# Kernel optimization log

Measured on AMD Instinct MI355X. Metric: run time of the kernel, lower is better.

Reference implementation:

```python
import jax, jax.numpy as jnp
import numpy as np

N_NODES = 50000   # local subgraph nodes
N_ENT   = 100000  # global entity vocab
N_REL   = 16
DIM     = 128
LAYERS  = 2
E       = 600000  # edges
Q       = 8192    # query triples
PATH_DIM = 5
RULE_INIT = [[1.0, 1.0, 0.5, 0.0, 0.0], [0.0, 0.0, 0.0, 1.0, 1.0]]


def setup_inputs() -> dict:
    key = jax.random.key(0)
    ks = jax.random.split(key, 11)
    node_ids   = jax.random.randint(ks[0], (N_NODES,), 0, N_ENT)
    edge_index = jax.random.randint(ks[1], (2, E), 0, N_NODES)
    edge_type  = jax.random.randint(ks[2], (E,), 0, N_REL)
    heads = jax.random.randint(ks[3], (Q,), 0, N_NODES)
    rels  = jax.random.randint(ks[4], (Q,), 0, N_REL)
    tails = jax.random.randint(ks[5], (Q,), 0, N_NODES)
    path_feat = jax.random.normal(ks[6], (Q, PATH_DIM), dtype=jnp.float32)
    # learned parameters
    entity_emb = jax.random.normal(ks[7], (N_ENT, DIM), dtype=jnp.float32) * 0.1
    rel_emb    = jax.random.normal(ks[8], (N_REL, DIM), dtype=jnp.float32) * 0.1
    W_self = jax.random.normal(ks[9], (LAYERS, DIM, DIM), dtype=jnp.float32) / np.sqrt(DIM)
    W_rel  = jax.random.normal(ks[10], (LAYERS, N_REL, DIM, DIM), dtype=jnp.float32) / np.sqrt(DIM)
    delta_weight = jnp.zeros((2, PATH_DIM), dtype=jnp.float32)
    lambda_logit = jnp.zeros((2,), dtype=jnp.float32)
    rule_init_weight = jnp.asarray(RULE_INIT, dtype=jnp.float32)
    return {
        'node_ids': node_ids, 'edge_index': edge_index, 'edge_type': edge_type,
        'heads': heads, 'rels': rels, 'tails': tails,
        'path_feat': path_feat, 'rel_task_idx': 0,
        'entity_emb': entity_emb, 'rel_emb': rel_emb,
        'W_self': W_self, 'W_rel': W_rel,
        'delta_weight': delta_weight, 'lambda_logit': lambda_logit,
        'rule_init_weight': rule_init_weight,
    }


def _rgcn_layer(h, Ws, Wr, src, dst, etype):
    # relation-specific transforms for all nodes: [R, N, D]
    h_rel = jnp.einsum('nd,rde->rne', h, Wr)
    msgs = h_rel[etype, src]                    # [E, D] gather per edge
    # per-(dst, relation) mean normalization (standard RGCN 1/c_{i,r})
    seg = dst * N_REL + etype
    cnt = jax.ops.segment_sum(jnp.ones((E,), h.dtype), seg, num_segments=N_NODES * N_REL)
    msgs = msgs / jnp.maximum(cnt[seg], 1.0)[:, None]
    agg = jax.ops.segment_sum(msgs, dst, num_segments=N_NODES)  # [N, D]
    return jax.nn.relu(h @ Ws + agg)


def reference(node_ids, edge_index, edge_type, heads, rels, tails, path_feat,
              rel_task_idx, entity_emb, rel_emb, W_self, W_rel,
              delta_weight, lambda_logit, rule_init_weight):
    src, dst = edge_index[0], edge_index[1]
    h = entity_emb[node_ids]                      # [N, D] local node states
    for l in range(LAYERS):
        h = _rgcn_layer(h, W_self[l], W_rel[l], src, dst, edge_type)
    # DistMult scoring of query triples (local indices)
    score_graph = jnp.sum(h[heads] * rel_emb[rels] * h[tails], axis=-1)  # [Q]
    # path branch
    final_weight = rule_init_weight[rel_task_idx] + delta_weight[rel_task_idx]  # [PATH_DIM]
    score_path = path_feat @ final_weight                                # [Q]
    lam = jax.nn.sigmoid(lambda_logit[rel_task_idx])
    return lam * score_graph + (1.0 - lam) * score_path
```

## Files before the change

kernel.cpp:

```cpp
#include <hip/hip_runtime.h>

#define N_NODES 50000
#define N_ENT   100000
#define N_REL   16
#define DIM     128
#define E_EDGES 600000
#define NQ      8192
#define PATH_DIM 5
#define NK      (N_NODES * N_REL)
#define NBLK_SEG (NK / 256)
#define KTOT    (N_REL * DIM + DIM)
#define NG      (KTOT / 32)
#define BM      64
#define EB      ((E_EDGES + 255) / 256)
#define H0B     ((N_NODES * 32) / 256)
#define WCB     ((2 * NG * 8 * 512) / 256)

typedef __attribute__((ext_vector_type(8))) short short8;
typedef __attribute__((ext_vector_type(4))) float floatx4;

static __device__ __forceinline__ short f2bf(float x) {
  unsigned u = __builtin_bit_cast(unsigned, x);
  u = (u + 0x7FFFu + ((u >> 16) & 1u)) >> 16;
  return (short)u;
}
static __device__ __forceinline__ float bf_lo(unsigned u) {
  return __builtin_bit_cast(float, u << 16);
}
static __device__ __forceinline__ float bf_hi(unsigned u) {
  return __builtin_bit_cast(float, u & 0xffff0000u);
}
static __device__ __forceinline__ unsigned pk2(float a, float b) {
  return (unsigned)(unsigned short)f2bf(a) | ((unsigned)(unsigned short)f2bf(b) << 16);
}

static __device__ __forceinline__ int wave_incl_scan(int x) {
  int lane = threadIdx.x & 63;
  #pragma unroll
  for (int off = 1; off < 64; off <<= 1) {
    int y = __shfl_up(x, off, 64);
    if (lane >= off) x += y;
  }
  return x;
}

static __device__ __forceinline__ unsigned gload_su(const unsigned* base, unsigned voff) {
  unsigned r;
  asm volatile("global_load_dword %0, %1, %2" : "=v"(r) : "v"(voff), "s"(base) : "memory");
  return r;
}
#define WAIT_VM(N) do { asm volatile("s_waitcnt vmcnt(" #N ")" ::: "memory"); \
                        __builtin_amdgcn_sched_barrier(0); } while (0)
#define BAR_LDS() do { asm volatile("s_waitcnt lgkmcnt(0)" ::: "memory"); \
                       __builtin_amdgcn_s_barrier(); \
                       asm volatile("" ::: "memory"); } while (0)

__global__ void k_prep(const int* __restrict__ ei, const int* __restrict__ et,
                       int* __restrict__ hist,
                       const int* __restrict__ nid, const float* __restrict__ emb,
                       unsigned* __restrict__ h,
                       const float* __restrict__ wrel, const float* __restrict__ wself,
                       short* __restrict__ wt) {
  int b = blockIdx.x, t = threadIdx.x;
  if (b < EB) {
    int e = b * 256 + t;
    if (e < E_EDGES) {
      int key = et[e] * N_NODES + ei[E_EDGES + e];
      atomicAdd(&hist[key], 1);
    }
  } else if (b < EB + H0B) {
    int g = (b - EB) * 256 + t;
    int n = g >> 5, q = g & 31;
    float4 v = *(const float4*)(emb + (size_t)nid[n] * DIM + q * 4);
    uint2 pk;
    pk.x = pk2(v.x, v.y);
    pk.y = pk2(v.z, v.w);
    *(uint2*)(h + (size_t)n * 64 + q * 2) = pk;
  } else {
    int idx = (b - EB - H0B) * 256 + t;
    int within = idx & 511;
    int tile = idx >> 9;
    int rA = within >> 5, q = within & 31;
    int nt8 = tile & 7;
    int lg = tile >> 3;
    int l = lg / NG, g = lg % NG;
    int n = nt8 * 16 + rA;
    int k = g * 32 + q;
    float v;
    if (k < N_REL * DIM) {
      int r = k >> 7, d = k & 127;
      v = wrel[(((size_t)l * N_REL + r) * DIM + d) * DIM + n];
    } else {
      int d = k - N_REL * DIM;
      v = wself[((size_t)l * DIM + d) * DIM + n];
    }
    wt[idx] = f2bf(v);
  }
}

__global__ void k_bsum(const int* __restrict__ hist, int* __restrict__ bsum) {
  int t = threadIdx.x;
  int v = hist[blockIdx.x * 256 + t];
  #pragma unroll
  for (int off = 32; off; off >>= 1) v += __shfl_xor(v, off, 64);
  __shared__ int s4[4];
  if ((t & 63) == 0) s4[t >> 6] = v;
  __syncthreads();
  if (t == 0) bsum[blockIdx.x] = s4[0] + s4[1] + s4[2] + s4[3];
}

__global__ void k_bscan(int* __restrict__ bsum) {
  int t = threadIdx.x;
  int v[4], loc[4], s = 0;
  #pragma unroll
  for (int i = 0; i < 4; i++) {
    int idx = t * 4 + i;
    v[i] = (idx < NBLK_SEG) ? bsum[idx] : 0;
    loc[i] = s; s += v[i];
  }
  int incl = wave_incl_scan(s);
  __shared__ int wsum[16];
  int wid = t >> 6, lane = t & 63;
  if (lane == 63) wsum[wid] = incl;
  __syncthreads();
  if (t < 16) {
    int x = wsum[t];
    #pragma unroll
    for (int off = 1; off < 16; off <<= 1) {
      int y = __shfl_up(x, off, 64);
      if (t >= off) x += y;
    }
    wsum[t] = x;
  }
  __syncthreads();
  int wexcl = wid ? wsum[wid - 1] : 0;
  int texcl = wexcl + incl - s;
  #pragma unroll
  for (int i = 0; i < 4; i++) {
    int idx = t * 4 + i;
    if (idx < NBLK_SEG) bsum[idx] = texcl + loc[i];
  }
}

__global__ void k_offsets(const int* __restrict__ hist, const int* __restrict__ bsum,
                          int* __restrict__ offs, int* __restrict__ cursor) {
  int t = threadIdx.x;
  int g = blockIdx.x * 256 + t;
  int v = hist[g];
  int incl = wave_incl_scan(v);
  __shared__ int wsum[4];
  int wid = t >> 6, lane = t & 63;
  if (lane == 63) wsum[wid] = incl;
  __syncthreads();
  int wexcl = 0;
  for (int i = 0; i < wid; i++) wexcl += wsum[i];
  int off = bsum[blockIdx.x] + wexcl + incl - v;
  offs[g] = off;
  cursor[g] = off;
  if (g == NK - 1) offs[NK] = off + v;
}

__global__ void k_scatter(const int* __restrict__ ei, const int* __restrict__ et,
                          int* __restrict__ cursor, int* __restrict__ ssrc) {
  int e = blockIdx.x * 256 + threadIdx.x;
  if (e >= E_EDGES) return;
  int src = ei[e];
  int key = et[e] * N_NODES + ei[E_EDGES + e];
  int pos = atomicAdd(&cursor[key], 1);
  ssrc[pos] = src;
}

__global__ __launch_bounds__(512, 4)
void k_layer(const unsigned* __restrict__ hin, const int* __restrict__ offs,
             const int* __restrict__ ssrc, const short* __restrict__ wt,
             unsigned* __restrict__ hout) {
  __shared__ unsigned As[2][BM][68];
  __shared__ int offsS[16][66];
  int t = threadIdx.x;
  int w = t >> 6, lane = t & 63;
  int row0 = blockIdx.x * BM;

  for (int idx = t; idx < 16 * 80; idx += 512) {
    int it = idx / 80, rr = idx - it * 80;
    if (rr < 65) offsS[it][rr] = offs[min(it * N_NODES + row0 + rr, NK)];
  }
  BAR_LDS();

  if (w < 4) {
    int w16 = w * 16;
    unsigned voffl = (unsigned)lane * 4u;
    unsigned uA[32], uB[32];
    int sjA, sjB;

    auto issue_sj = [&](int r) -> int {
      int o0 = offsS[r][w16];
      unsigned vo = (unsigned)min(o0 + lane, E_EDGES - 1) * 4u;
      return (int)gload_su((const unsigned*)ssrc, vo);
    };
    auto issue_u = [&](unsigned (&u)[32], int sjv) {
      #pragma unroll
      for (int e = 0; e < 32; ++e) {
        int sr = __builtin_amdgcn_readlane(sjv, e);
        u[e] = gload_su(hin + (size_t)sr * 64, voffl);
      }
    };
    auto accum = [&](unsigned (&u)[32], int r) {
      int olv = offsS[r][w16 + min(lane, 16)];
      int o0 = __builtin_amdgcn_readfirstlane(olv);
      int total = __builtin_amdgcn_readlane(olv, 16) - o0;
      int nxt = __shfl(olv, lane + 1);
      int cnl = nxt - olv;
      float ivf = 1.0f / (float)(cnl > 0 ? cnl : 1);
      int ivb = __builtin_bit_cast(int, ivf);
      int k = 0;
      int nb = __builtin_amdgcn_readlane(olv, 1) - o0;
      float r0 = 0.f, r1 = 0.f;
      int buf = r & 1;
      auto close1 = [&]() {
        float f = __builtin_bit_cast(float, __builtin_amdgcn_readlane(ivb, k));
        float a = r0 * f, b2 = r1 * f;
        unsigned pk;
        asm("v_cvt_pk_bf16_f32 %0, %1, %2" : "=v"(pk) : "v"(a), "v"(b2));
        As[buf][w16 + k][lane] = pk;
        r0 = 0.f; r1 = 0.f;
        ++k;
        nb = __builtin_amdgcn_readlane(olv, min(k + 1, 16)) - o0;
      };
      #pragma unroll
      for (int e = 0; e < 32; ++e) {
        while (k < 16 && nb == e) close1();
        if (e < total) { r0 += bf_lo(u[e]); r1 += bf_hi(u[e]); }
      }
      if (total > 32) {
        for (int e = 32; e < total; ++e) {
          while (k < 16 && nb == e) close1();
          int sr = __builtin_amdgcn_readfirstlane(ssrc[o0 + e]);
          unsigned uu = hin[(size_t)sr * 64 + lane];
          r0 += bf_lo(uu); r1 += bf_hi(uu);
        }
      }
      while (k < 16) close1();
    };

    sjA = issue_sj(0);
    WAIT_VM(0);
    sjB = issue_sj(1);
    issue_u(uA, sjA);
    WAIT_VM(32);
    sjA = issue_sj(2);
    issue_u(uB, sjB);
    WAIT_VM(33);
    accum(uA, 0);
    BAR_LDS();

    auto phase = [&](int p, unsigned (&uI)[32], unsigned (&uAcc)[32],
                     int &sjC, int &sjN) {
      WAIT_VM(32);
      sjN = issue_sj(min(p + 3, 15));
      issue_u(uI, sjC);
      WAIT_VM(33);
      accum(uAcc, p + 1);
      BAR_LDS();
    };
    for (int p = 0; p < 15; p += 2) {
      phase(p, uA, uB, sjA, sjB);
      if (p + 1 < 15) phase(p + 1, uB, uA, sjB, sjA);
    }

    #pragma unroll
    for (int j = 0; j < 16; ++j) {
      int lr = min(row0 + w16 + j, N_NODES - 1);
      As[0][w16 + j][lane] = hin[(size_t)lr * 64 + lane];
    }
    BAR_LDS();
  } else {
    int wid = w - 4, wm = wid >> 1, wn = wid & 1;
    int quad = lane >> 4, rA = lane & 15;
    floatx4 acc[2][4];
    #pragma unroll
    for (int a = 0; a < 2; a++)
      #pragma unroll
      for (int b = 0; b < 4; b++) acc[a][b] = (floatx4)0.f;

    BAR_LDS();
    for (int it = 0; it < 17; ++it) {
      int buf = it & 1;
      const short* arow0 = (const short*)&As[buf][wm * 32 + rA][0];
      const short* arow1 = (const short*)&As[buf][wm * 32 + 16 + rA][0];
      #pragma unroll
      for (int ks = 0; ks < 4; ++ks) {
        short8 a0 = *(const short8*)(arow0 + ks * 32 + quad * 8);
        short8 a1 = *(const short8*)(arow1 + ks * 32 + quad * 8);
        int kg = it * 4 + ks;
        const short* bp = wt + (size_t)(kg * 8 + wn * 4) * 512 + rA * 32 + quad * 8;
        #pragma unroll
        for (int nt = 0; nt < 4; ++nt) {
          short8 b = *(const short8*)(bp + nt * 512);
          acc[0][nt] = __builtin_amdgcn_mfma_f32_16x16x32_bf16(a0, b, acc[0][nt], 0, 0, 0);
          acc[1][nt] = __builtin_amdgcn_mfma_f32_16x16x32_bf16(a1, b, acc[1][nt], 0, 0, 0);
        }
      }
      if (it < 16) BAR_LDS();
    }
    #pragma unroll
    for (int mt = 0; mt < 2; ++mt)
      #pragma unroll
      for (int nt = 0; nt < 4; ++nt)
        #pragma unroll
        for (int j = 0; j < 4; ++j) {
          int row = row0 + wm * 32 + mt * 16 + quad * 4 + j;
          int col = wn * 64 + nt * 16 + rA;
          if (row < N_NODES)
            ((short*)hout)[(size_t)row * DIM + col] = f2bf(fmaxf(acc[mt][nt][j], 0.f));
        }
  }
}

__global__ void k_score(const unsigned* __restrict__ h, const int* __restrict__ heads,
                        const int* __restrict__ rels, const int* __restrict__ tails,
                        const float* __restrict__ rel_emb, const float* __restrict__ path_feat,
                        const int* __restrict__ task_idx, const float* __restrict__ delta_w,
                        const float* __restrict__ lambda_logit, const float* __restrict__ rule_init,
                        float* __restrict__ out) {
  int q = (blockIdx.x * 256 + threadIdx.x) >> 6;
  int lane = threadIdx.x & 63;
  int hd = heads[q], tl = tails[q], rl = rels[q];
  unsigned ua = h[(size_t)hd * 64 + lane];
  unsigned uc = h[(size_t)tl * 64 + lane];
  float2 r = *(const float2*)(rel_emb + (size_t)rl * DIM + lane * 2);
  float s = bf_lo(ua) * r.x * bf_lo(uc) + bf_hi(ua) * r.y * bf_hi(uc);
  #pragma unroll
  for (int off = 32; off; off >>= 1) s += __shfl_xor(s, off, 64);
  if (lane == 0) {
    int task = task_idx[0];
    float sp = 0.f;
    #pragma unroll
    for (int p = 0; p < PATH_DIM; p++)
      sp += path_feat[q * PATH_DIM + p] *
            (rule_init[task * PATH_DIM + p] + delta_w[task * PATH_DIM + p]);
    float lam = 1.f / (1.f + __expf(-lambda_logit[task]));
    out[q] = lam * s + (1.f - lam) * sp;
  }
}

extern "C" void kernel_launch(void* const* d_in, const int* in_sizes, int n_in,
                              void* d_out, int out_size, void* d_ws, size_t ws_size,
                              hipStream_t stream) {
  const int*   node_ids   = (const int*)d_in[0];
  const int*   edge_index = (const int*)d_in[1];
  const int*   edge_type  = (const int*)d_in[2];
  const int*   heads      = (const int*)d_in[3];
  const int*   rels       = (const int*)d_in[4];
  const int*   tails      = (const int*)d_in[5];
  const float* path_feat  = (const float*)d_in[6];
  const int*   task_idx   = (const int*)d_in[7];
  const float* entity_emb = (const float*)d_in[8];
  const float* rel_emb    = (const float*)d_in[9];
  const float* W_self     = (const float*)d_in[10];
  const float* W_rel      = (const float*)d_in[11];
  const float* delta_w    = (const float*)d_in[12];
  const float* lambda_lg  = (const float*)d_in[13];
  const float* rule_init  = (const float*)d_in[14];

  char* ws = (char*)d_ws;
  size_t off = 0;
  auto alloc = [&](size_t bytes) -> void* {
    void* p = ws + off;
    off = (off + bytes + 255) & ~(size_t)255;
    return p;
  };
  unsigned* h_a    = (unsigned*)alloc((size_t)N_NODES * DIM * 2);
  unsigned* h_b    = (unsigned*)alloc((size_t)N_NODES * DIM * 2);
  short*    wt     = (short*)alloc((size_t)2 * NG * 8 * 512 * 2);
  int*      offs   = (int*)alloc((size_t)(NK + 1) * 4);
  int*      ssrc   = (int*)alloc((size_t)E_EDGES * 4);
  int*      hist   = (int*)alloc((size_t)(NK + 1) * 4);
  int*      cursor = (int*)alloc((size_t)NK * 4);
  int*      bsum   = (int*)alloc((size_t)NBLK_SEG * 4);

  hipMemsetAsync(hist, 0, (size_t)(NK + 1) * 4, stream);
  k_prep<<<EB + H0B + WCB, 256, 0, stream>>>(edge_index, edge_type, hist,
                                             node_ids, entity_emb, h_a,
                                             W_rel, W_self, wt);
  k_bsum<<<NBLK_SEG, 256, 0, stream>>>(hist, bsum);
  k_bscan<<<1, 1024, 0, stream>>>(bsum);
  k_offsets<<<NBLK_SEG, 256, 0, stream>>>(hist, bsum, offs, cursor);
  k_scatter<<<EB, 256, 0, stream>>>(edge_index, edge_type, cursor, ssrc);

  const unsigned* hin = h_a;
  unsigned* hout = h_b;
  int nblk = (N_NODES + BM - 1) / BM;
  for (int l = 0; l < 2; l++) {
    k_layer<<<nblk, 512, 0, stream>>>(hin, offs, ssrc,
                                      wt + (size_t)l * NG * 8 * 512, hout);
    const unsigned* tmp = hout;
    hout = (unsigned*)hin;
    hin = tmp;
  }
  k_score<<<NQ / 4, 256, 0, stream>>>(hin, heads, rels, tails, rel_emb, path_feat,
                                      task_idx, delta_w, lambda_lg, rule_init,
                                      (float*)d_out);
}
```

Before: 442.7 us.

## Unify gather and MFMA waves, stage edge gathers directly into LDS

Replaces the producer/consumer warp specialization (4 gather waves, 4 MFMA waves, double-buffered A tile) with all 8 waves doing both gather-aggregation of 8 rows and MFMA on a 16x64 output tile. Neighbor source indices and row gathers now go through global_load_lds into per-wave LDS buffers (13 edges per phase) instead of register arrays, cutting register pressure. The aim is more gather parallelism and occupancy. In exchange, gather and MFMA phases now serialize within each wave behind barriers, and a smaller edge prefetch window means more rows fall back to the slow scalar-load path.

```diff
diff --git a/kernel.cpp b/kernel.cpp
--- a/kernel.cpp
+++ b/kernel.cpp
@@ -12,6 +12,7 @@
 #define KTOT    (N_REL * DIM + DIM)
 #define NG      (KTOT / 32)
 #define BM      64
+#define EMAX    13
 #define EB      ((E_EDGES + 255) / 256)
 #define H0B     ((N_NODES * 32) / 256)
 #define WCB     ((2 * NG * 8 * 512) / 256)
@@ -44,16 +45,13 @@
   return x;
 }
 
-static __device__ __forceinline__ unsigned gload_su(const unsigned* base, unsigned voff) {
-  unsigned r;
-  asm volatile("global_load_dword %0, %1, %2" : "=v"(r) : "v"(voff), "s"(base) : "memory");
-  return r;
-}
-#define WAIT_VM(N) do { asm volatile("s_waitcnt vmcnt(" #N ")" ::: "memory"); \
-                        __builtin_amdgcn_sched_barrier(0); } while (0)
+#define GLOAD_LDS4(g, l) __builtin_amdgcn_global_load_lds(                     \
+    (const __attribute__((address_space(1))) void*)(g),                        \
+    (__attribute__((address_space(3))) void*)(l), 4, 0, 0)
+#define SB() __builtin_amdgcn_sched_barrier(0)
+#define WAIT_VM(N) do { asm volatile("s_waitcnt vmcnt(" #N ")" ::: "memory"); SB(); } while (0)
 #define BAR_LDS() do { asm volatile("s_waitcnt lgkmcnt(0)" ::: "memory"); \
-                       __builtin_amdgcn_s_barrier(); \
-                       asm volatile("" ::: "memory"); } while (0)
+                       __builtin_amdgcn_s_barrier(); SB(); } while (0)
 
 __global__ void k_prep(const int* __restrict__ ei, const int* __restrict__ et,
                        int* __restrict__ hist,
@@ -174,10 +172,15 @@
 void k_layer(const unsigned* __restrict__ hin, const int* __restrict__ offs,
              const int* __restrict__ ssrc, const short* __restrict__ wt,
              unsigned* __restrict__ hout) {
-  __shared__ unsigned As[2][BM][68];
+  __shared__ unsigned As[BM][68];
+  __shared__ unsigned ebuf[8][2][EMAX][64];
+  __shared__ int jbuf[8][2][64];
   __shared__ int offsS[16][66];
   int t = threadIdx.x;
   int w = t >> 6, lane = t & 63;
+  int quad = lane >> 4, rA = lane & 15;
+  int w8 = w * 8;
+  int wm16 = (w >> 1) * 16, wn4 = (w & 1) * 4;
   int row0 = blockIdx.x * BM;
 
   for (int idx = t; idx < 16 * 80; idx += 512) {
@@ -186,134 +189,124 @@
   }
   BAR_LDS();
 
-  if (w < 4) {
-    int w16 = w * 16;
-    unsigned voffl = (unsigned)lane * 4u;
-    unsigned uA[32], uB[32];
-    int sjA, sjB;
-
-    auto issue_sj = [&](int r) -> int {
-      int o0 = offsS[r][w16];
-      unsigned vo = (unsigned)min(o0 + lane, E_EDGES - 1) * 4u;
-      return (int)gload_su((const unsigned*)ssrc, vo);
+  floatx4 acc[4];
+  #pragma unroll
+  for (int nt = 0; nt < 4; ++nt) acc[nt] = (floatx4)0.f;
+
+  auto issue_j = [&](int p, int jb) {
+    int o0 = offsS[min(p, 15)][w8];
+    GLOAD_LDS4(ssrc + min(o0 + lane, E_EDGES - 1), &jbuf[w][jb][0]);
+  };
+  auto issue_s = [&](int p) {
+    int bix = p & 1;
+    #pragma unroll
+    for (int e = 0; e < EMAX; ++e) {
+      int sid = jbuf[w][bix][e];
+      GLOAD_LDS4(hin + (size_t)sid * 64 + lane, &ebuf[w][bix][e][0]);
+    }
+  };
+  auto accum_f = [&](int p) {
+    int bix = p & 1;
+    int olv = offsS[p][w8 + min(lane, 8)];
+    int o0 = __builtin_amdgcn_readfirstlane(olv);
+    int total = __builtin_amdgcn_readlane(olv, 8) - o0;
+    int nxt = __shfl(olv, lane + 1, 64);
+    int cnl = nxt - olv;
+    float ivf = 1.0f / (float)(cnl > 0 ? cnl : 1);
+    int ivb = __builtin_bit_cast(int, ivf);
+    int k = 0;
+    int nb = __builtin_amdgcn_readlane(olv, 1) - o0;
+    float r0 = 0.f, r1 = 0.f;
+    auto close1 = [&]() {
+      float f = __builtin_bit_cast(float, __builtin_amdgcn_readlane(ivb, k));
+      float a = r0 * f, b = r1 * f;
+      unsigned pk;
+      asm("v_cvt_pk_bf16_f32 %0, %1, %2" : "=v"(pk) : "v"(a), "v"(b));
+      As[w8 + k][lane] = pk;
+      r0 = 0.f; r1 = 0.f;
+      ++k;
+      nb = __builtin_amdgcn_readlane(olv, min(k + 1, 8)) - o0;
     };
-    auto issue_u = [&](unsigned (&u)[32], int sjv) {
+    #pragma unroll
+    for (int e = 0; e < EMAX; ++e) {
+      while (k < 8 && nb == e) close1();
+      if (e < total) {
+        unsigned uv = ebuf[w][bix][e][lane];
+        r0 += bf_lo(uv); r1 += bf_hi(uv);
+      }
+    }
+    if (total > EMAX) {
+      for (int e = EMAX; e < total; ++e) {
+        while (k < 8 && nb == e) close1();
+        int sr = __builtin_amdgcn_readfirstlane(ssrc[o0 + e]);
+        unsigned uu = hin[(size_t)sr * 64 + lane];
+        r0 += bf_lo(uu); r1 += bf_hi(uu);
+      }
+    }
+    while (k < 8) close1();
+  };
+  auto do_mfma = [&](int p) {
+    const short* arow = (const short*)&As[wm16 + rA][0];
+    #pragma unroll
+    for (int ks = 0; ks < 4; ++ks) {
+      short8 a0 = *(const short8*)(arow + ks * 32 + quad * 8);
+      int kg = p * 4 + ks;
+      const short* bp = wt + (size_t)(kg * 8 + wn4) * 512 + rA * 32 + quad * 8;
       #pragma unroll
-      for (int e = 0; e < 32; ++e) {
-        int sr = __builtin_amdgcn_readlane(sjv, e);
-        u[e] = gload_su(hin + (size_t)sr * 64, voffl);
+      for (int nt = 0; nt < 4; ++nt) {
+        short8 b = *(const short8*)(bp + nt * 512);
+        acc[nt] = __builtin_amdgcn_mfma_f32_16x16x32_bf16(a0, b, acc[nt], 0, 0, 0);
       }
-    };
-    auto accum = [&](unsigned (&u)[32], int r) {
-      int olv = offsS[r][w16 + min(lane, 16)];
-      int o0 = __builtin_amdgcn_readfirstlane(olv);
-      int total = __builtin_amdgcn_readlane(olv, 16) - o0;
-      int nxt = __shfl(olv, lane + 1);
-      int cnl = nxt - olv;
-      float ivf = 1.0f / (float)(cnl > 0 ? cnl : 1);
-      int ivb = __builtin_bit_cast(int, ivf);
-      int k = 0;
-      int nb = __builtin_amdgcn_readlane(olv, 1) - o0;
-      float r0 = 0.f, r1 = 0.f;
-      int buf = r & 1;
-      auto close1 = [&]() {
-        float f = __builtin_bit_cast(float, __builtin_amdgcn_readlane(ivb, k));
-        float a = r0 * f, b2 = r1 * f;
-        unsigned pk;
-        asm("v_cvt_pk_bf16_f32 %0, %1, %2" : "=v"(pk) : "v"(a), "v"(b2));
-        As[buf][w16 + k][lane] = pk;
-        r0 = 0.f; r1 = 0.f;
-        ++k;
-        nb = __builtin_amdgcn_readlane(olv, min(k + 1, 16)) - o0;
-      };
-      #pragma unroll
-      for (int e = 0; e < 32; ++e) {
-        while (k < 16 && nb == e) close1();
-        if (e < total) { r0 += bf_lo(u[e]); r1 += bf_hi(u[e]); }
-      }
-      if (total > 32) {
-        for (int e = 32; e < total; ++e) {
-          while (k < 16 && nb == e) close1();
-          int sr = __builtin_amdgcn_readfirstlane(ssrc[o0 + e]);
-          unsigned uu = hin[(size_t)sr * 64 + lane];
-          r0 += bf_lo(uu); r1 += bf_hi(uu);
-        }
-      }
-      while (k < 16) close1();
-    };
-
-    sjA = issue_sj(0);
-    WAIT_VM(0);
-    sjB = issue_sj(1);
-    issue_u(uA, sjA);
-    WAIT_VM(32);
-    sjA = issue_sj(2);
-    issue_u(uB, sjB);
-    WAIT_VM(33);
-    accum(uA, 0);
+    }
+  };
+
+  issue_j(0, 0);
+  WAIT_VM(0);
+  issue_j(1, 1);
+  SB();
+  issue_s(0);
+  SB();
+  WAIT_VM(13);
+  issue_j(2, 0);
+  SB();
+  issue_s(1);
+  SB();
+  WAIT_VM(14);
+  accum_f(0);
+  BAR_LDS();
+  do_mfma(0);
+  BAR_LDS();
+
+  for (int p = 1; p <= 15; ++p) {
+    WAIT_VM(13);
+    issue_j(p + 2, p & 1);
+    SB();
+    issue_s(p + 1);
+    SB();
+    WAIT_VM(14);
+    accum_f(p);
     BAR_LDS();
-
-    auto phase = [&](int p, unsigned (&uI)[32], unsigned (&uAcc)[32],
-                     int &sjC, int &sjN) {
-      WAIT_VM(32);
-      sjN = issue_sj(min(p + 3, 15));
-      issue_u(uI, sjC);
-      WAIT_VM(33);
-      accum(uAcc, p + 1);
-      BAR_LDS();
-    };
-    for (int p = 0; p < 15; p += 2) {
-      phase(p, uA, uB, sjA, sjB);
-      if (p + 1 < 15) phase(p + 1, uB, uA, sjB, sjA);
-    }
-
-    #pragma unroll
-    for (int j = 0; j < 16; ++j) {
-      int lr = min(row0 + w16 + j, N_NODES - 1);
-      As[0][w16 + j][lane] = hin[(size_t)lr * 64 + lane];
-    }
+    do_mfma(p);
     BAR_LDS();
-  } else {
-    int wid = w - 4, wm = wid >> 1, wn = wid & 1;
-    int quad = lane >> 4, rA = lane & 15;
-    floatx4 acc[2][4];
-    #pragma unroll
-    for (int a = 0; a < 2; a++)
-      #pragma unroll
-      for (int b = 0; b < 4; b++) acc[a][b] = (floatx4)0.f;
-
-    BAR_LDS();
-    for (int it = 0; it < 17; ++it) {
-      int buf = it & 1;
-      const short* arow0 = (const short*)&As[buf][wm * 32 + rA][0];
-      const short* arow1 = (const short*)&As[buf][wm * 32 + 16 + rA][0];
-      #pragma unroll
-      for (int ks = 0; ks < 4; ++ks) {
-        short8 a0 = *(const short8*)(arow0 + ks * 32 + quad * 8);
-        short8 a1 = *(const short8*)(arow1 + ks * 32 + quad * 8);
-        int kg = it * 4 + ks;
-        const short* bp = wt + (size_t)(kg * 8 + wn * 4) * 512 + rA * 32 + quad * 8;
-        #pragma unroll
-        for (int nt = 0; nt < 4; ++nt) {
-          short8 b = *(const short8*)(bp + nt * 512);
-          acc[0][nt] = __builtin_amdgcn_mfma_f32_16x16x32_bf16(a0, b, acc[0][nt], 0, 0, 0);
-          acc[1][nt] = __builtin_amdgcn_mfma_f32_16x16x32_bf16(a1, b, acc[1][nt], 0, 0, 0);
-        }
-      }
-      if (it < 16) BAR_LDS();
-    }
-    #pragma unroll
-    for (int mt = 0; mt < 2; ++mt)
-      #pragma unroll
-      for (int nt = 0; nt < 4; ++nt)
-        #pragma unroll
-        for (int j = 0; j < 4; ++j) {
-          int row = row0 + wm * 32 + mt * 16 + quad * 4 + j;
-          int col = wn * 64 + nt * 16 + rA;
-          if (row < N_NODES)
-            ((short*)hout)[(size_t)row * DIM + col] = f2bf(fmaxf(acc[mt][nt][j], 0.f));
-        }
-  }
+  }
+
+  #pragma unroll
+  for (int j = 0; j < 8; ++j) {
+    int lr = min(row0 + w8 + j, N_NODES - 1);
+    As[w8 + j][lane] = hin[(size_t)lr * 64 + lane];
+  }
+  BAR_LDS();
+  do_mfma(16);
+
+  #pragma unroll
+  for (int nt = 0; nt < 4; ++nt)
+    #pragma unroll
+    for (int j = 0; j < 4; ++j) {
+      int row = row0 + wm16 + quad * 4 + j;
+      int col = (w & 1) * 64 + nt * 16 + rA;
+      if (row < N_NODES)
+        ((short*)hout)[(size_t)row * DIM + col] = f2bf(fmaxf(acc[nt][j], 0.f));
+    }
 }
 
 __global__ void k_score(const unsigned* __restrict__ h, const int* __restrict__ heads,
```

After: 561.3 us. +26.8%, slower.
